# Kernel optimization log

Measured on AMD Instinct MI355X. Metric: run time of the kernel, lower is better.

## Reference

```python
import jax, jax.numpy as jnp
import numpy as np

IN_DIM = 768
ATT_DIM = 512
N_HEADS = 8
HEAD_DIM = ATT_DIM // N_HEADS


def setup_inputs() -> dict:
    key = jax.random.key(0)
    k1, k2, k3 = jax.random.split(key, 3)
    X = jax.random.normal(k1, (4, 2048, IN_DIM), dtype=jnp.float32)
    # qkv linear (no bias): weight [3*att_dim, in_dim], torch convention y = x W^T
    W_qkv = jax.random.normal(k2, (3 * ATT_DIM, IN_DIM), dtype=jnp.float32) * (1.0 / np.sqrt(IN_DIM))
    W_out = jax.random.normal(k3, (IN_DIM, ATT_DIM), dtype=jnp.float32) * (1.0 / np.sqrt(ATT_DIM))
    b_out = jnp.zeros((IN_DIM,), dtype=jnp.float32)
    return {"X": X, "W_qkv": W_qkv, "W_out": W_out, "b_out": b_out}


def reference(X, W_qkv, W_out, b_out):
    b, n, _ = X.shape
    QKV = jnp.einsum('bnf,cf->bnc', X, W_qkv)  # [b, n, 3*att_dim]
    # rearrange 'b n (p h d) -> p b h n d'
    QKV = QKV.reshape(b, n, 3, N_HEADS, HEAD_DIM).transpose(2, 0, 3, 1, 4)
    Q, K, V = QKV[0], QKV[1], QKV[2]  # each [b, h, n, d]
    scores = jnp.einsum('bhid,bhjd->bhij', Q, K) / np.sqrt(HEAD_DIM)
    A = jax.nn.softmax(scores, axis=-1)  # dropout p=0 -> identity
    Y = jnp.einsum('bhij,bhjd->bhid', A, V)
    Y = Y.transpose(0, 2, 1, 3).reshape(b, n, ATT_DIM)  # 'b h n d -> b n (h d)'
    return jnp.einsum('bna,oa->bno', Y, W_out) + b_out
```

## Files before the change

kernel.cpp:

```cpp
#include <hip/hip_runtime.h>

typedef __bf16 bf16;
typedef unsigned int u32;
typedef __attribute__((ext_vector_type(8))) __bf16 bf16x8;
typedef __attribute__((ext_vector_type(4))) __bf16 bf16x4;
typedef __attribute__((ext_vector_type(4))) float floatx4;

#define IN_DIM  768
#define ATT_DIM 512
#define NH      8
#define HD      64
#define BATCH   4
#define SEQ     2048
#define M_TOT   (BATCH*SEQ)
#define QKV_N   (3*ATT_DIM)

#define QSCALE 0.18033688011112042f

__device__ __forceinline__ void cp16(void* lds, const void* g) {
    __builtin_amdgcn_global_load_lds((const __attribute__((address_space(1))) u32*)g,
                                     (__attribute__((address_space(3))) u32*)lds, 16, 0, 0);
}
__device__ __forceinline__ const bf16* swz(const bf16* b, int row, int chunk) {
    return b + row * 64 + (((chunk) ^ (row & 7)) << 3);
}

#define N8_X  (M_TOT * IN_DIM / 8)
#define N8_WQ (QKV_N * IN_DIM / 8)
#define N8_WO (IN_DIM * ATT_DIM / 8)
#define N8_ALL (N8_X + N8_WQ + N8_WO)

__global__ __launch_bounds__(256) void cvt_all(const float* __restrict__ X,
                                               const float* __restrict__ Wq,
                                               const float* __restrict__ Wo,
                                               bf16* __restrict__ Xb,
                                               bf16* __restrict__ Wqb,
                                               bf16* __restrict__ Wob) {
    int i = blockIdx.x * 256 + threadIdx.x;
    const float* s; bf16* d; int off;
    if (i < N8_X)            { s = X;  d = Xb;  off = i; }
    else if (i < N8_X+N8_WQ) { s = Wq; d = Wqb; off = i - N8_X; }
    else                     { s = Wo; d = Wob; off = i - N8_X - N8_WQ; }
    const float4 a = ((const float4*)s)[2*off];
    const float4 b = ((const float4*)s)[2*off+1];
    bf16x8 o = {(bf16)a.x,(bf16)a.y,(bf16)a.z,(bf16)a.w,
                (bf16)b.x,(bf16)b.y,(bf16)b.z,(bf16)b.w};
    ((bf16x8*)d)[off] = o;
}

__global__ __launch_bounds__(256) void qkv_gemm(const bf16* __restrict__ Xb,
                                                const bf16* __restrict__ Wb,
                                                bf16* __restrict__ Q,
                                                bf16* __restrict__ Kv,
                                                bf16* __restrict__ VT) {
    __shared__ __align__(16) char smraw[34816];
    bf16* As = (bf16*)smraw;
    bf16* Bs = (bf16*)(smraw + 16384);

    const int tid  = threadIdx.x;
    const int bm0  = blockIdx.y * 128;
    const int bn0  = blockIdx.x * 128;
    const int wave = tid >> 6, lane = tid & 63;
    const int quad = lane >> 4, l15 = lane & 15;
    const int wm = (wave >> 1) * 64, wn = (wave & 1) * 64;
    const int r8 = lane >> 3, cc = (lane & 7) ^ r8;

    const bf16* ag = Xb + (size_t)(bm0 + wave * 32 + r8) * IN_DIM + cc * 8;
    const bf16* bg = Wb + (size_t)(bn0 + wave * 32 + r8) * IN_DIM + cc * 8;

    floatx4 acc[4][4];
#pragma unroll
    for (int i = 0; i < 4; ++i)
#pragma unroll
        for (int j = 0; j < 4; ++j) acc[i][j] = (floatx4){0.f, 0.f, 0.f, 0.f};

    for (int kt = 0; kt < IN_DIM / 64; ++kt) {
        __syncthreads();
#pragma unroll
        for (int it = 0; it < 4; ++it) {
            cp16(&As[(wave * 32 + it * 8) * 64], ag + it * (8 * IN_DIM) + kt * 64);
            cp16(&Bs[(wave * 32 + it * 8) * 64], bg + it * (8 * IN_DIM) + kt * 64);
        }
        __syncthreads();

        bf16x8 af[2][4], bfr[2][4];
#pragma unroll
        for (int kh = 0; kh < 2; ++kh)
#pragma unroll
            for (int i = 0; i < 4; ++i) {
                af[kh][i]  = *(const bf16x8*)swz(As, wm + i * 16 + l15, kh * 4 + quad);
                bfr[kh][i] = *(const bf16x8*)swz(Bs, wn + i * 16 + l15, kh * 4 + quad);
            }
#pragma unroll
        for (int kh = 0; kh < 2; ++kh)
#pragma unroll
            for (int i = 0; i < 4; ++i)
#pragma unroll
                for (int j = 0; j < 4; ++j)
                    acc[i][j] = __builtin_amdgcn_mfma_f32_16x16x32_bf16(af[kh][i], bfr[kh][j], acc[i][j], 0, 0, 0);
    }

    const int b = bm0 >> 11, nbase = bm0 & 2047;

    if (bn0 < 1024) {
#pragma unroll
        for (int i = 0; i < 4; ++i)
#pragma unroll
            for (int j = 0; j < 4; ++j)
#pragma unroll
                for (int r = 0; r < 4; ++r) {
                    const int row = bm0 + wm + i * 16 + quad * 4 + r;
                    const int col = bn0 + wn + j * 16 + l15;
                    const float v = acc[i][j][r];
                    const int rem = col & 511;
                    const int h = rem >> 6, d = rem & 63;
                    const int n = row & 2047;
                    const size_t idx = (((size_t)((row >> 11) * NH + h)) * SEQ + n) * HD + d;
                    if (col < 512) Q[idx]  = (bf16)(v * QSCALE);
                    else           Kv[idx] = (bf16)v;
                }
    } else {
        __syncthreads();
        bf16 (*Ts)[136] = (bf16(*)[136])smraw;
#pragma unroll
        for (int i = 0; i < 4; ++i)
#pragma unroll
            for (int j = 0; j < 4; ++j) {
                bf16x4 pk = {(bf16)acc[i][j][0], (bf16)acc[i][j][1],
                             (bf16)acc[i][j][2], (bf16)acc[i][j][3]};
                *(bf16x4*)&Ts[wn + j * 16 + l15][wm + i * 16 + quad * 4] = pk;
            }
        __syncthreads();
        const int cb = bn0 - 1024;
#pragma unroll
        for (int t2 = 0; t2 < 8; ++t2) {
            const int id = tid + t2 * 256;
            const int c = id >> 4, nc = (id & 15) * 8;
            const int col = cb + c;
            const int h = col >> 6, d = col & 63;
            *(bf16x8*)&VT[(((size_t)(b * NH + h)) * HD + d) * SEQ + nbase + nc] =
                *(const bf16x8*)&Ts[c][nc];
        }
    }
}

__global__ __launch_bounds__(256, 4) void attn(const bf16* __restrict__ Q,
                                               const bf16* __restrict__ K,
                                               const bf16* __restrict__ VT,
                                               bf16* __restrict__ Y) {
    __shared__ bf16 Ks[2][64 * 64];
    __shared__ bf16 VTs[64 * 64];
    __shared__ bf16 PsT[4][16 * 72];

    const int tid  = threadIdx.x;
    const int wave = tid >> 6, lane = tid & 63;
    const int quad = lane >> 4, l15 = lane & 15;
    const int bh = blockIdx.x;
    const int q0 = blockIdx.y * 64;
    const bf16* Qg = Q  + (size_t)bh * SEQ * HD;
    const bf16* Kg = K  + (size_t)bh * SEQ * HD;
    const bf16* Vg = VT + (size_t)bh * HD * SEQ;

    const int r8 = lane >> 3, cc = (lane & 7) ^ r8;

    bf16x8 aq[2];
    aq[0] = *(const bf16x8*)&Qg[(size_t)(q0 + wave * 16 + l15) * 64 + quad * 8];
    aq[1] = *(const bf16x8*)&Qg[(size_t)(q0 + wave * 16 + l15) * 64 + 32 + quad * 8];

    const bf16* kg0 = Kg + (size_t)(wave * 16 + r8) * 64 + cc * 8;
    const bf16* kg1 = Kg + (size_t)(wave * 16 + 8 + r8) * 64 + cc * 8;
    const bf16* vg0 = Vg + (size_t)(wave * 16 + r8) * 2048 + cc * 8;
    const bf16* vg1 = Vg + (size_t)(wave * 16 + 8 + r8) * 2048 + cc * 8;

    cp16(&Ks[0][(wave * 16) * 64], kg0);
    cp16(&Ks[0][(wave * 16 + 8) * 64], kg1);

    float l = 0.f;
    floatx4 o[4];
#pragma unroll
    for (int db = 0; db < 4; ++db) o[db] = (floatx4){0.f, 0.f, 0.f, 0.f};

    bf16* psw = &PsT[wave][0];

    for (int kt = 0; kt < SEQ / 64; ++kt) {
        const int cur = kt & 1;
        __syncthreads();
        cp16(&VTs[(wave * 16) * 64], vg0 + kt * 64);
        cp16(&VTs[(wave * 16 + 8) * 64], vg1 + kt * 64);
        if (kt < SEQ / 64 - 1) {
            cp16(&Ks[cur ^ 1][(wave * 16) * 64], kg0 + (size_t)(kt + 1) * 4096);
            cp16(&Ks[cur ^ 1][(wave * 16 + 8) * 64], kg1 + (size_t)(kt + 1) * 4096);
        }

#pragma unroll
        for (int t = 0; t < 4; ++t) {
            const int kr = t * 16 + l15;
            const bf16x8 k0 = *(const bf16x8*)swz(Ks[cur], kr, quad);
            const bf16x8 k1 = *(const bf16x8*)swz(Ks[cur], kr, 4 + quad);
            floatx4 z = (floatx4){0.f, 0.f, 0.f, 0.f};
            z = __builtin_amdgcn_mfma_f32_16x16x32_bf16(k0, aq[0], z, 0, 0, 0);
            z = __builtin_amdgcn_mfma_f32_16x16x32_bf16(k1, aq[1], z, 0, 0, 0);
            const float p0 = __builtin_amdgcn_exp2f(z[0]);
            const float p1 = __builtin_amdgcn_exp2f(z[1]);
            const float p2 = __builtin_amdgcn_exp2f(z[2]);
            const float p3 = __builtin_amdgcn_exp2f(z[3]);
            l += (p0 + p1) + (p2 + p3);
            bf16x4 pk = {(bf16)p0, (bf16)p1, (bf16)p2, (bf16)p3};
            *(bf16x4*)&psw[l15 * 72 + t * 16 + quad * 4] = pk;
        }
        const bf16x8 pa0 = *(const bf16x8*)&psw[l15 * 72 + quad * 8];
        const bf16x8 pa1 = *(const bf16x8*)&psw[l15 * 72 + 32 + quad * 8];

        __syncthreads();

#pragma unroll
        for (int db = 0; db < 4; ++db) {
            const int vr = db * 16 + l15;
            const bf16x8 v0 = *(const bf16x8*)swz(VTs, vr, quad);
            const bf16x8 v1 = *(const bf16x8*)swz(VTs, vr, 4 + quad);
            o[db] = __builtin_amdgcn_mfma_f32_16x16x32_bf16(pa0, v0, o[db], 0, 0, 0);
            o[db] = __builtin_amdgcn_mfma_f32_16x16x32_bf16(pa1, v1, o[db], 0, 0, 0);
        }
    }

    l += __shfl_xor(l, 16, 64);
    l += __shfl_xor(l, 32, 64);
    const float inv = 1.0f / l;
    float linv[4];
#pragma unroll
    for (int r = 0; r < 4; ++r)
        linv[r] = __int_as_float(__builtin_amdgcn_ds_bpermute((quad * 4 + r) * 4,
                                                              __float_as_int(inv)));
    const int b = bh >> 3, h = bh & 7;
#pragma unroll
    for (int db = 0; db < 4; ++db)
#pragma unroll
        for (int r = 0; r < 4; ++r) {
            const int n = q0 + wave * 16 + quad * 4 + r;
            Y[((size_t)(b * SEQ + n)) * ATT_DIM + h * HD + db * 16 + l15] =
                (bf16)(o[db][r] * linv[r]);
        }
}

__global__ __launch_bounds__(256) void out_gemm(const bf16* __restrict__ Yb,
                                                const bf16* __restrict__ Wb,
                                                const float* __restrict__ bias,
                                                float* __restrict__ out) {
    __shared__ __align__(16) bf16 As[128 * 64];
    __shared__ __align__(16) bf16 Bs[128 * 64];

    const int tid  = threadIdx.x;
    const int bm0  = blockIdx.y * 128;
    const int bn0  = blockIdx.x * 128;
    const int wave = tid >> 6, lane = tid & 63;
    const int quad = lane >> 4, l15 = lane & 15;
    const int wm = (wave >> 1) * 64, wn = (wave & 1) * 64;
    const int r8 = lane >> 3, cc = (lane & 7) ^ r8;

    const bf16* ag = Yb + (size_t)(bm0 + wave * 32 + r8) * ATT_DIM + cc * 8;
    const bf16* bg = Wb + (size_t)(bn0 + wave * 32 + r8) * ATT_DIM + cc * 8;

    floatx4 acc[4][4];
#pragma unroll
    for (int i = 0; i < 4; ++i)
#pragma unroll
        for (int j = 0; j < 4; ++j) acc[i][j] = (floatx4){0.f, 0.f, 0.f, 0.f};

    for (int kt = 0; kt < ATT_DIM / 64; ++kt) {
        __syncthreads();
#pragma unroll
        for (int it = 0; it < 4; ++it) {
            cp16(&As[(wave * 32 + it * 8) * 64], ag + it * (8 * ATT_DIM) + kt * 64);
            cp16(&Bs[(wave * 32 + it * 8) * 64], bg + it * (8 * ATT_DIM) + kt * 64);
        }
        __syncthreads();

        bf16x8 af[2][4], bfr[2][4];
#pragma unroll
        for (int kh = 0; kh < 2; ++kh)
#pragma unroll
            for (int i = 0; i < 4; ++i) {
                af[kh][i]  = *(const bf16x8*)swz(As, wm + i * 16 + l15, kh * 4 + quad);
                bfr[kh][i] = *(const bf16x8*)swz(Bs, wn + i * 16 + l15, kh * 4 + quad);
            }
#pragma unroll
        for (int kh = 0; kh < 2; ++kh)
#pragma unroll
            for (int i = 0; i < 4; ++i)
#pragma unroll
                for (int j = 0; j < 4; ++j)
                    acc[i][j] = __builtin_amdgcn_mfma_f32_16x16x32_bf16(af[kh][i], bfr[kh][j], acc[i][j], 0, 0, 0);
    }

#pragma unroll
    for (int i = 0; i < 4; ++i)
#pragma unroll
        for (int j = 0; j < 4; ++j)
#pragma unroll
            for (int r = 0; r < 4; ++r) {
                const int row = bm0 + wm + i * 16 + quad * 4 + r;
                const int col = bn0 + wn + j * 16 + l15;
                out[(size_t)row * IN_DIM + col] = acc[i][j][r] + bias[col];
            }
}

extern "C" void kernel_launch(void* const* d_in, const int* in_sizes, int n_in,
                              void* d_out, int out_size, void* d_ws, size_t ws_size,
                              hipStream_t stream) {
    const float* X    = (const float*)d_in[0];
    const float* Wqkv = (const float*)d_in[1];
    const float* Wout = (const float*)d_in[2];
    const float* bout = (const float*)d_in[3];
    float* out = (float*)d_out;

    char* ws = (char*)d_ws;
    size_t off = 0;
    bf16* Xb  = (bf16*)(ws + off); off += (size_t)M_TOT * IN_DIM * 2;
    bf16* Wqb = (bf16*)(ws + off); off += (size_t)QKV_N * IN_DIM * 2;
    bf16* Wob = (bf16*)(ws + off); off += (size_t)IN_DIM * ATT_DIM * 2;
    const size_t T = (size_t)BATCH * NH * SEQ * HD * 2;
    bf16* Q  = (bf16*)(ws + off); off += T;
    bf16* K  = (bf16*)(ws + off); off += T;
    bf16* VT = (bf16*)(ws + off); off += T;
    bf16* Y  = (bf16*)(ws + off); off += T;

    cvt_all<<<N8_ALL / 256, 256, 0, stream>>>(X, Wqkv, Wout, Xb, Wqb, Wob);
    qkv_gemm<<<dim3(QKV_N / 128, M_TOT / 128), 256, 0, stream>>>(Xb, Wqb, Q, K, VT);
    attn<<<dim3(BATCH * NH, SEQ / 64), 256, 0, stream>>>(Q, K, VT, Y);
    out_gemm<<<dim3(IN_DIM / 128, M_TOT / 128), 256, 0, stream>>>(Y, Wob, bout, out);
}
```

Before: 179.2 us.

## Double-buffer V tiles and drop mid-loop barrier in attention kernel

V^T tiles now get double-buffered the same way K tiles already are: the next V tile is prefetched at the start of each iteration, so the second __syncthreads per iteration can be removed. The per-wave P staging buffer moves from a padded 72-stride layout to an XOR-swizzled 64-stride layout to avoid bank conflicts on the write and read. The cost is more LDS per block, which may limit occupancy. Correctness now depends on the load-to-LDS completing before the single remaining barrier, without a separate wait.

After: 176.9 us. Within noise of the previous version (-1.3%).

```diff
diff --git a/kernel.cpp b/kernel.cpp
--- a/kernel.cpp
+++ b/kernel.cpp
@@ -149,8 +149,8 @@
                                                const bf16* __restrict__ VT,
                                                bf16* __restrict__ Y) {
     __shared__ bf16 Ks[2][64 * 64];
-    __shared__ bf16 VTs[64 * 64];
-    __shared__ bf16 PsT[4][16 * 72];
+    __shared__ bf16 VTs[2][64 * 64];
+    __shared__ bf16 Ps[4][16 * 64];
 
     const int tid  = threadIdx.x;
     const int wave = tid >> 6, lane = tid & 63;
@@ -174,22 +174,24 @@
 
     cp16(&Ks[0][(wave * 16) * 64], kg0);
     cp16(&Ks[0][(wave * 16 + 8) * 64], kg1);
+    cp16(&VTs[0][(wave * 16) * 64], vg0);
+    cp16(&VTs[0][(wave * 16 + 8) * 64], vg1);
 
     float l = 0.f;
     floatx4 o[4];
 #pragma unroll
     for (int db = 0; db < 4; ++db) o[db] = (floatx4){0.f, 0.f, 0.f, 0.f};
 
-    bf16* psw = &PsT[wave][0];
+    bf16* psw = &Ps[wave][0];
 
     for (int kt = 0; kt < SEQ / 64; ++kt) {
-        const int cur = kt & 1;
-        __syncthreads();
-        cp16(&VTs[(wave * 16) * 64], vg0 + kt * 64);
-        cp16(&VTs[(wave * 16 + 8) * 64], vg1 + kt * 64);
+        const int cur = kt & 1, nb = cur ^ 1;
+        __syncthreads();
         if (kt < SEQ / 64 - 1) {
-            cp16(&Ks[cur ^ 1][(wave * 16) * 64], kg0 + (size_t)(kt + 1) * 4096);
-            cp16(&Ks[cur ^ 1][(wave * 16 + 8) * 64], kg1 + (size_t)(kt + 1) * 4096);
+            cp16(&Ks[nb][(wave * 16) * 64], kg0 + (size_t)(kt + 1) * 4096);
+            cp16(&Ks[nb][(wave * 16 + 8) * 64], kg1 + (size_t)(kt + 1) * 4096);
+            cp16(&VTs[nb][(wave * 16) * 64], vg0 + (kt + 1) * 64);
+            cp16(&VTs[nb][(wave * 16 + 8) * 64], vg1 + (kt + 1) * 64);
         }
 
 #pragma unroll
@@ -206,18 +208,17 @@
             const float p3 = __builtin_amdgcn_exp2f(z[3]);
             l += (p0 + p1) + (p2 + p3);
             bf16x4 pk = {(bf16)p0, (bf16)p1, (bf16)p2, (bf16)p3};
-            *(bf16x4*)&psw[l15 * 72 + t * 16 + quad * 4] = pk;
-        }
-        const bf16x8 pa0 = *(const bf16x8*)&psw[l15 * 72 + quad * 8];
-        const bf16x8 pa1 = *(const bf16x8*)&psw[l15 * 72 + 32 + quad * 8];
-
-        __syncthreads();
+            const int c = t * 2 + (quad >> 1);
+            *(bf16x4*)&psw[l15 * 64 + ((c ^ (l15 & 7)) << 3) + ((quad & 1) << 2)] = pk;
+        }
+        const bf16x8 pa0 = *(const bf16x8*)swz(psw, l15, quad);
+        const bf16x8 pa1 = *(const bf16x8*)swz(psw, l15, 4 + quad);
 
 #pragma unroll
         for (int db = 0; db < 4; ++db) {
             const int vr = db * 16 + l15;
-            const bf16x8 v0 = *(const bf16x8*)swz(VTs, vr, quad);
-            const bf16x8 v1 = *(const bf16x8*)swz(VTs, vr, 4 + quad);
+            const bf16x8 v0 = *(const bf16x8*)swz(VTs[cur], vr, quad);
+            const bf16x8 v1 = *(const bf16x8*)swz(VTs[cur], vr, 4 + quad);
             o[db] = __builtin_amdgcn_mfma_f32_16x16x32_bf16(pa0, v0, o[db], 0, 0, 0);
             o[db] = __builtin_amdgcn_mfma_f32_16x16x32_bf16(pa1, v1, o[db], 0, 0, 0);
         }
```
